# Optimization experiments

Hardware: AMD Instinct MI355X
Metric: run time of the kernel (lower is better)

The kernel has to match this reference:

```python
import jax, jax.numpy as jnp
import numpy as np
from jax import lax

EPS = 1e-6
NUM_BANDS = 128


def setup_inputs() -> dict:
    key = jax.random.key(0)
    kx, = jax.random.split(key, 1)
    B, C, F, T = 32, 1, NUM_BANDS, 6000
    x = jax.random.uniform(kx, (B, C, F, T), dtype=jnp.float32)  # nonneg spectrogram energies
    # parameters per band, initialized as in PCEN.__init__ (s=0.025, alpha=delta=r=1.0)
    log_s = jnp.full((F,), np.log(0.025), dtype=jnp.float32)
    log_alpha = jnp.zeros((F,), dtype=jnp.float32)
    log_delta = jnp.zeros((F,), dtype=jnp.float32)
    log_r = jnp.zeros((F,), dtype=jnp.float32)
    return {"x": x, "log_s": log_s, "log_alpha": log_alpha,
            "log_delta": log_delta, "log_r": log_r}


def _pcen(x, log_s, log_alpha, log_delta, log_r):
    # x: (B, C, bands, T)
    s = jnp.exp(log_s)  # (bands,)
    xt = jnp.moveaxis(x, -1, 0)  # (T, B, C, bands) time-major for the scan
    init = xt[0]  # init_smoother_from_data=True -> M_0 = X_0

    def step(m, xf):
        m_new = (1.0 - s) * m + s * xf
        return m_new, m_new

    _, ms = lax.scan(step, init, xt[1:])  # (T-1, B, C, bands)
    smoother = jnp.concatenate([init[None], ms], axis=0)  # (T, B, C, bands)
    smoother = jnp.moveaxis(smoother, 0, -1)  # (B, C, bands, T)

    alpha = jnp.exp(log_alpha)[:, None]  # (bands, 1)
    delta = jnp.exp(log_delta)[:, None]
    r = jnp.exp(log_r)[:, None]
    # (eps + M)^(-alpha) computed stably: exp(-alpha * (log eps + log1p(M/eps)))
    gain = jnp.exp(-alpha * (jnp.log(EPS) + jnp.log1p(smoother / EPS)))
    return (x * gain + delta) ** r - delta ** r


def reference(x, log_s, log_alpha, log_delta, log_r):
    return _pcen(x, log_s, log_alpha, log_delta, log_r)
```

## Files before the change

### kernel.cpp

```cpp
#include <hip/hip_runtime.h>

#define TLEN     6000
#define NV4      1500
#define CHUNK_V4 256
#define HALF_V4  768
#define EPS      1e-6f
#define LN_EPS   (-13.815511f)
#define INV_EPS  1e6f

__device__ __forceinline__ float pcen_full(float xv, float M, float alpha,
                                           float delta, float r, float deltar) {
    float gain = __expf(-alpha * (LN_EPS + __logf(fmaf(M, INV_EPS, 1.0f))));
    return __powf(fmaf(xv, gain, delta), r) - deltar;
}

__device__ __forceinline__ float ipow6(float b, int e) {
    float r = 1.0f;
    #pragma unroll
    for (int i = 0; i < 6; ++i) {
        if (e & 1) r *= b;
        b *= b;
        e >>= 1;
    }
    return r;
}

template<bool PARTIAL>
__device__ __forceinline__ float chunk_compute(
    const float4 (&q)[4], const int fb, const int lane, const bool finit,
    const float s, const float oms, const float omsP, const float Apow,
    const float A64, const bool triv,
    const float la, const float ld, const float lr,
    const float Mc, float4* __restrict__ ob)
{
    float B = 0.0f;
    #pragma unroll
    for (int j = 0; j < 4; ++j) {
        if (!PARTIAL || (fb + j < NV4)) {
            const float c0 = (finit && lane == 0 && j == 0) ? 1.0f : s;
            B = fmaf(oms, B, c0 * q[j].x);
            B = fmaf(oms, B, s  * q[j].y);
            B = fmaf(oms, B, s  * q[j].z);
            B = fmaf(oms, B, s  * q[j].w);
        }
    }

    float S = B;
    float w = omsP;
    #pragma unroll
    for (int off = 1; off < 64; off <<= 1) {
        const float Sp = __shfl_up(S, off, 64);
        if (lane >= off) S = fmaf(w, Sp, S);
        w *= w;
    }
    const float Se  = __shfl_up(S, 1, 64);
    const float Be  = (lane == 0) ? 0.0f : Se;
    const float Min = fmaf(Apow, Mc, Be);

    float McNext = 0.0f;
    if (!PARTIAL) McNext = fmaf(A64, Mc, __shfl(S, 63, 64));

    float m = Min;
    if (triv) {
        #pragma unroll
        for (int j = 0; j < 4; ++j) {
            if (!PARTIAL || (fb + j < NV4)) {
                const float c0 = (finit && lane == 0 && j == 0) ? 1.0f : s;
                float4 o;
                m = fmaf(oms, m, c0 * q[j].x); o.x = q[j].x * __builtin_amdgcn_rcpf(m + EPS);
                m = fmaf(oms, m, s  * q[j].y); o.y = q[j].y * __builtin_amdgcn_rcpf(m + EPS);
                m = fmaf(oms, m, s  * q[j].z); o.z = q[j].z * __builtin_amdgcn_rcpf(m + EPS);
                m = fmaf(oms, m, s  * q[j].w); o.w = q[j].w * __builtin_amdgcn_rcpf(m + EPS);
                ob[fb + j] = o;
            }
        }
    } else {
        const float alpha  = __expf(la);
        const float delta  = __expf(ld);
        const float r      = __expf(lr);
        const float deltar = __powf(delta, lr == 0.0f ? 1.0f : r);
        #pragma unroll
        for (int j = 0; j < 4; ++j) {
            if (!PARTIAL || (fb + j < NV4)) {
                const float c0 = (finit && lane == 0 && j == 0) ? 1.0f : s;
                float4 o;
                m = fmaf(oms, m, c0 * q[j].x); o.x = pcen_full(q[j].x, m, alpha, delta, r, deltar);
                m = fmaf(oms, m, s  * q[j].y); o.y = pcen_full(q[j].y, m, alpha, delta, r, deltar);
                m = fmaf(oms, m, s  * q[j].z); o.z = pcen_full(q[j].z, m, alpha, delta, r, deltar);
                m = fmaf(oms, m, s  * q[j].w); o.w = pcen_full(q[j].w, m, alpha, delta, r, deltar);
                ob[fb + j] = o;
            }
        }
    }
    return McNext;
}

__global__ __launch_bounds__(256, 4) void pcen_kernel(
    const float* __restrict__ x,
    const float* __restrict__ log_s,
    const float* __restrict__ log_alpha,
    const float* __restrict__ log_delta,
    const float* __restrict__ log_r,
    float* __restrict__ out,
    int num_series, int F)
{
    const int g    = (int)((blockIdx.x * blockDim.x + threadIdx.x) >> 6);
    const int lane = (int)(threadIdx.x & 63);
    if (g >= num_series * 2) return;
    const int series = g >> 1;
    const int h      = g & 1;
    const int f      = series % F;

    const float la = log_alpha[f], ld = log_delta[f], lr = log_r[f];
    const bool  triv = (la == 0.0f) && (ld == 0.0f) && (lr == 0.0f);

    const float s    = __expf(log_s[f]);
    const float oms  = 1.0f - s;
    const float oms2 = oms * oms;
    const float oms4 = oms2 * oms2;
    const float oms8 = oms4 * oms4;
    const float omsP = oms8 * oms8;

    float A64 = omsP;
    #pragma unroll
    for (int i = 0; i < 6; ++i) A64 *= A64;
    const bool decay_ok = fabsf(A64) < 1e-7f;

    const float Apow = ipow6(omsP, lane);

    const float4* __restrict__ xb = (const float4*)(x + (size_t)series * TLEN);
    float4* __restrict__ ob       = (float4*)(out + (size_t)series * TLEN);

    const int hb = h * HALF_V4;
    const int l4 = 4 * lane;

    float4 bufA[4], bufB[4];

    #pragma unroll
    for (int j = 0; j < 4; ++j) bufA[j] = xb[hb + l4 + j];

    float Mc = 0.0f;
    if (h == 1) {
        const float wl = ipow6(omsP, 63 - lane);
        if (decay_ok) {
            #pragma unroll
            for (int j = 0; j < 4; ++j) bufB[j] = xb[(HALF_V4 - CHUNK_V4) + l4 + j];
            float Bw = 0.0f;
            #pragma unroll
            for (int j = 0; j < 4; ++j) {
                const float4 qw = bufB[j];
                Bw = fmaf(oms, Bw, s * qw.x);
                Bw = fmaf(oms, Bw, s * qw.y);
                Bw = fmaf(oms, Bw, s * qw.z);
                Bw = fmaf(oms, Bw, s * qw.w);
            }
            float v = wl * Bw;
            #pragma unroll
            for (int off = 1; off < 64; off <<= 1) v += __shfl_xor(v, off, 64);
            Mc = v;
        } else {
            for (int wc = 0; wc < 3; ++wc) {
                float Bw = 0.0f;
                #pragma unroll
                for (int j = 0; j < 4; ++j) {
                    const float4 qw = xb[wc * CHUNK_V4 + l4 + j];
                    const float c0 = (wc == 0 && lane == 0 && j == 0) ? 1.0f : s;
                    Bw = fmaf(oms, Bw, c0 * qw.x);
                    Bw = fmaf(oms, Bw, s  * qw.y);
                    Bw = fmaf(oms, Bw, s  * qw.z);
                    Bw = fmaf(oms, Bw, s  * qw.w);
                }
                float v = wl * Bw;
                #pragma unroll
                for (int off = 1; off < 64; off <<= 1) v += __shfl_xor(v, off, 64);
                Mc = fmaf(A64, Mc, v);
            }
        }
    }

    #pragma unroll
    for (int j = 0; j < 4; ++j) bufB[j] = xb[hb + CHUNK_V4 + l4 + j];

    Mc = chunk_compute<false>(bufA, hb + l4, lane, (h == 0),
                              s, oms, omsP, Apow, A64, triv, la, ld, lr, Mc, ob);

    {
        const int fb2 = hb + 2 * CHUNK_V4 + l4;
        #pragma unroll
        for (int j = 0; j < 4; ++j)
            bufA[j] = (fb2 + j < NV4) ? xb[fb2 + j] : make_float4(0.f, 0.f, 0.f, 0.f);
    }

    Mc = chunk_compute<false>(bufB, hb + CHUNK_V4 + l4, lane, false,
                              s, oms, omsP, Apow, A64, triv, la, ld, lr, Mc, ob);

    chunk_compute<true>(bufA, hb + 2 * CHUNK_V4 + l4, lane, false,
                        s, oms, omsP, Apow, A64, triv, la, ld, lr, Mc, ob);
}

extern "C" void kernel_launch(void* const* d_in, const int* in_sizes, int n_in,
                              void* d_out, int out_size, void* d_ws, size_t ws_size,
                              hipStream_t stream) {
    const float* x         = (const float*)d_in[0];
    const float* log_s     = (const float*)d_in[1];
    const float* log_alpha = (const float*)d_in[2];
    const float* log_delta = (const float*)d_in[3];
    const float* log_r     = (const float*)d_in[4];
    float* out             = (float*)d_out;

    const int F = in_sizes[1];
    const int num_series = in_sizes[0] / TLEN;
    const int num_waves  = num_series * 2;
    const int num_threads = num_waves * 64;
    const int grid = (num_threads + 255) / 256;

    pcen_kernel<<<grid, 256, 0, stream>>>(x, log_s, log_alpha, log_delta, log_r,
                                          out, num_series, F);
}
```

Before: 191.2 us.

## Interleave float4 loads across lanes and run four parallel wave scans per chunk

Each lane now loads float4 elements strided by 64 (lane-contiguous across the wave) instead of four consecutive float4s per lane, so every warp load instruction touches one contiguous 1 KB span. The per-chunk scan becomes four independent 64-lane shuffle scans with decay oms^4, chained serially through the carry Mc with A256. Gain parameters are hoisted out of the chunk function. This trades more shuffle work (four scans instead of one) for fully coalesced memory access and shorter serial per-lane recurrences.

Result: faster. 182.9 us (-4.3%).

```diff
diff --git a/kernel.cpp b/kernel.cpp
--- a/kernel.cpp
+++ b/kernel.cpp
@@ -3,6 +3,7 @@
 #define TLEN     6000
 #define NV4      1500
 #define CHUNK_V4 256
+#define SUB_V4   64
 #define HALF_V4  768
 #define EPS      1e-6f
 #define LN_EPS   (-13.815511f)
@@ -27,72 +28,76 @@
 
 template<bool PARTIAL>
 __device__ __forceinline__ float chunk_compute(
-    const float4 (&q)[4], const int fb, const int lane, const bool finit,
-    const float s, const float oms, const float omsP, const float Apow,
-    const float A64, const bool triv,
-    const float la, const float ld, const float lr,
-    const float Mc, float4* __restrict__ ob)
+    const float4 (&q)[4], const int cb, const int lane, const bool finit,
+    const float s, const float oms, const float oms4, const float Apow4,
+    const float A256, const bool triv,
+    const float alpha, const float delta, const float r, const float deltar,
+    float Mc, float4* __restrict__ ob)
 {
-    float B = 0.0f;
+    float B[4];
     #pragma unroll
     for (int j = 0; j < 4; ++j) {
-        if (!PARTIAL || (fb + j < NV4)) {
-            const float c0 = (finit && lane == 0 && j == 0) ? 1.0f : s;
-            B = fmaf(oms, B, c0 * q[j].x);
-            B = fmaf(oms, B, s  * q[j].y);
-            B = fmaf(oms, B, s  * q[j].z);
-            B = fmaf(oms, B, s  * q[j].w);
-        }
-    }
-
-    float S = B;
-    float w = omsP;
+        const float c0 = (finit && j == 0 && lane == 0) ? 1.0f : s;
+        float b = c0 * q[j].x;
+        b = fmaf(oms, b, s * q[j].y);
+        b = fmaf(oms, b, s * q[j].z);
+        b = fmaf(oms, b, s * q[j].w);
+        B[j] = b;
+    }
+
+    float S[4];
+    #pragma unroll
+    for (int j = 0; j < 4; ++j) S[j] = B[j];
+    float w = oms4;
     #pragma unroll
     for (int off = 1; off < 64; off <<= 1) {
-        const float Sp = __shfl_up(S, off, 64);
-        if (lane >= off) S = fmaf(w, Sp, S);
+        #pragma unroll
+        for (int j = 0; j < 4; ++j) {
+            const float Sp = __shfl_up(S[j], off, 64);
+            if (lane >= off) S[j] = fmaf(w, Sp, S[j]);
+        }
         w *= w;
     }
-    const float Se  = __shfl_up(S, 1, 64);
-    const float Be  = (lane == 0) ? 0.0f : Se;
-    const float Min = fmaf(Apow, Mc, Be);
-
-    float McNext = 0.0f;
-    if (!PARTIAL) McNext = fmaf(A64, Mc, __shfl(S, 63, 64));
-
-    float m = Min;
+
+    float Min[4];
+    #pragma unroll
+    for (int j = 0; j < 4; ++j) {
+        const float Se = __shfl_up(S[j], 1, 64);
+        const float Be = (lane == 0) ? 0.0f : Se;
+        Min[j] = fmaf(Apow4, Mc, Be);
+        Mc = fmaf(A256, Mc, __shfl(S[j], 63, 64));
+    }
+
     if (triv) {
         #pragma unroll
         for (int j = 0; j < 4; ++j) {
-            if (!PARTIAL || (fb + j < NV4)) {
-                const float c0 = (finit && lane == 0 && j == 0) ? 1.0f : s;
-                float4 o;
+            const int vi = cb + SUB_V4 * j + lane;
+            if (!PARTIAL || vi < NV4) {
+                const float c0 = (finit && j == 0 && lane == 0) ? 1.0f : s;
+                float m = Min[j]; float4 o;
                 m = fmaf(oms, m, c0 * q[j].x); o.x = q[j].x * __builtin_amdgcn_rcpf(m + EPS);
                 m = fmaf(oms, m, s  * q[j].y); o.y = q[j].y * __builtin_amdgcn_rcpf(m + EPS);
                 m = fmaf(oms, m, s  * q[j].z); o.z = q[j].z * __builtin_amdgcn_rcpf(m + EPS);
                 m = fmaf(oms, m, s  * q[j].w); o.w = q[j].w * __builtin_amdgcn_rcpf(m + EPS);
-                ob[fb + j] = o;
+                ob[vi] = o;
             }
         }
     } else {
-        const float alpha  = __expf(la);
-        const float delta  = __expf(ld);
-        const float r      = __expf(lr);
-        const float deltar = __powf(delta, lr == 0.0f ? 1.0f : r);
         #pragma unroll
         for (int j = 0; j < 4; ++j) {
-            if (!PARTIAL || (fb + j < NV4)) {
-                const float c0 = (finit && lane == 0 && j == 0) ? 1.0f : s;
-                float4 o;
+            const int vi = cb + SUB_V4 * j + lane;
+            if (!PARTIAL || vi < NV4) {
+                const float c0 = (finit && j == 0 && lane == 0) ? 1.0f : s;
+                float m = Min[j]; float4 o;
                 m = fmaf(oms, m, c0 * q[j].x); o.x = pcen_full(q[j].x, m, alpha, delta, r, deltar);
                 m = fmaf(oms, m, s  * q[j].y); o.y = pcen_full(q[j].y, m, alpha, delta, r, deltar);
                 m = fmaf(oms, m, s  * q[j].z); o.z = pcen_full(q[j].z, m, alpha, delta, r, deltar);
                 m = fmaf(oms, m, s  * q[j].w); o.w = pcen_full(q[j].w, m, alpha, delta, r, deltar);
-                ob[fb + j] = o;
-            }
-        }
-    }
-    return McNext;
+                ob[vi] = o;
+            }
+        }
+    }
+    return Mc;
 }
 
 __global__ __launch_bounds__(256, 4) void pcen_kernel(
@@ -118,84 +123,93 @@
     const float oms  = 1.0f - s;
     const float oms2 = oms * oms;
     const float oms4 = oms2 * oms2;
-    const float oms8 = oms4 * oms4;
-    const float omsP = oms8 * oms8;
-
-    float A64 = omsP;
-    #pragma unroll
-    for (int i = 0; i < 6; ++i) A64 *= A64;
-    const bool decay_ok = fabsf(A64) < 1e-7f;
-
-    const float Apow = ipow6(omsP, lane);
+
+    float A256 = oms4;
+    #pragma unroll
+    for (int i = 0; i < 6; ++i) A256 *= A256;
+    float A1024 = A256 * A256; A1024 *= A1024;
+    const bool decay_ok = fabsf(A1024) < 1e-7f;
+
+    const float Apow4 = ipow6(oms4, lane);
+
+    float alpha = 0.f, delta = 0.f, rr = 0.f, deltar = 0.f;
+    if (!triv) {
+        alpha  = __expf(la);
+        delta  = __expf(ld);
+        rr     = __expf(lr);
+        deltar = __powf(delta, lr == 0.0f ? 1.0f : rr);
+    }
 
     const float4* __restrict__ xb = (const float4*)(x + (size_t)series * TLEN);
     float4* __restrict__ ob       = (float4*)(out + (size_t)series * TLEN);
 
     const int hb = h * HALF_V4;
-    const int l4 = 4 * lane;
 
     float4 bufA[4], bufB[4];
 
     #pragma unroll
-    for (int j = 0; j < 4; ++j) bufA[j] = xb[hb + l4 + j];
+    for (int j = 0; j < 4; ++j) bufA[j] = xb[hb + SUB_V4 * j + lane];
 
     float Mc = 0.0f;
     if (h == 1) {
-        const float wl = ipow6(omsP, 63 - lane);
+        const float wl = ipow6(oms4, 63 - lane);
         if (decay_ok) {
             #pragma unroll
-            for (int j = 0; j < 4; ++j) bufB[j] = xb[(HALF_V4 - CHUNK_V4) + l4 + j];
-            float Bw = 0.0f;
+            for (int j = 0; j < 4; ++j) bufB[j] = xb[(HALF_V4 - CHUNK_V4) + SUB_V4 * j + lane];
+            float Bw[4];
             #pragma unroll
             for (int j = 0; j < 4; ++j) {
-                const float4 qw = bufB[j];
-                Bw = fmaf(oms, Bw, s * qw.x);
-                Bw = fmaf(oms, Bw, s * qw.y);
-                Bw = fmaf(oms, Bw, s * qw.z);
-                Bw = fmaf(oms, Bw, s * qw.w);
-            }
-            float v = wl * Bw;
+                float b = s * bufB[j].x;
+                b = fmaf(oms, b, s * bufB[j].y);
+                b = fmaf(oms, b, s * bufB[j].z);
+                b = fmaf(oms, b, s * bufB[j].w);
+                Bw[j] = b;
+            }
+            float v = wl * fmaf(A256, fmaf(A256, fmaf(A256, Bw[0], Bw[1]), Bw[2]), Bw[3]);
             #pragma unroll
             for (int off = 1; off < 64; off <<= 1) v += __shfl_xor(v, off, 64);
             Mc = v;
         } else {
             for (int wc = 0; wc < 3; ++wc) {
-                float Bw = 0.0f;
+                float Bw[4];
                 #pragma unroll
                 for (int j = 0; j < 4; ++j) {
-                    const float4 qw = xb[wc * CHUNK_V4 + l4 + j];
-                    const float c0 = (wc == 0 && lane == 0 && j == 0) ? 1.0f : s;
-                    Bw = fmaf(oms, Bw, c0 * qw.x);
-                    Bw = fmaf(oms, Bw, s  * qw.y);
-                    Bw = fmaf(oms, Bw, s  * qw.z);
-                    Bw = fmaf(oms, Bw, s  * qw.w);
+                    const float4 qw = xb[wc * CHUNK_V4 + SUB_V4 * j + lane];
+                    const float c0 = (wc == 0 && j == 0 && lane == 0) ? 1.0f : s;
+                    float b = c0 * qw.x;
+                    b = fmaf(oms, b, s * qw.y);
+                    b = fmaf(oms, b, s * qw.z);
+                    b = fmaf(oms, b, s * qw.w);
+                    Bw[j] = b;
                 }
-                float v = wl * Bw;
+                float v = wl * fmaf(A256, fmaf(A256, fmaf(A256, Bw[0], Bw[1]), Bw[2]), Bw[3]);
                 #pragma unroll
                 for (int off = 1; off < 64; off <<= 1) v += __shfl_xor(v, off, 64);
-                Mc = fmaf(A64, Mc, v);
-            }
-        }
-    }
-
-    #pragma unroll
-    for (int j = 0; j < 4; ++j) bufB[j] = xb[hb + CHUNK_V4 + l4 + j];
-
-    Mc = chunk_compute<false>(bufA, hb + l4, lane, (h == 0),
-                              s, oms, omsP, Apow, A64, triv, la, ld, lr, Mc, ob);
-
-    {
-        const int fb2 = hb + 2 * CHUNK_V4 + l4;
-        #pragma unroll
-        for (int j = 0; j < 4; ++j)
-            bufA[j] = (fb2 + j < NV4) ? xb[fb2 + j] : make_float4(0.f, 0.f, 0.f, 0.f);
-    }
-
-    Mc = chunk_compute<false>(bufB, hb + CHUNK_V4 + l4, lane, false,
-                              s, oms, omsP, Apow, A64, triv, la, ld, lr, Mc, ob);
-
-    chunk_compute<true>(bufA, hb + 2 * CHUNK_V4 + l4, lane, false,
-                        s, oms, omsP, Apow, A64, triv, la, ld, lr, Mc, ob);
+                Mc = fmaf(A1024, Mc, v);
+            }
+        }
+    }
+
+    #pragma unroll
+    for (int j = 0; j < 4; ++j) bufB[j] = xb[hb + CHUNK_V4 + SUB_V4 * j + lane];
+
+    Mc = chunk_compute<false>(bufA, hb, lane, (h == 0),
+                              s, oms, oms4, Apow4, A256, triv,
+                              alpha, delta, rr, deltar, Mc, ob);
+
+    #pragma unroll
+    for (int j = 0; j < 4; ++j) {
+        const int vi = hb + 2 * CHUNK_V4 + SUB_V4 * j + lane;
+        bufA[j] = (vi < NV4) ? xb[vi] : make_float4(0.f, 0.f, 0.f, 0.f);
+    }
+
+    Mc = chunk_compute<false>(bufB, hb + CHUNK_V4, lane, false,
+                              s, oms, oms4, Apow4, A256, triv,
+                              alpha, delta, rr, deltar, Mc, ob);
+
+    chunk_compute<true>(bufA, hb + 2 * CHUNK_V4, lane, false,
+                        s, oms, oms4, Apow4, A256, triv,
+                        alpha, delta, rr, deltar, Mc, ob);
 }
 
 extern "C" void kernel_launch(void* const* d_in, const int* in_sizes, int n_in,
```
